# Performance work log

Hardware: AMD Instinct MI355X
Metric: run time of the kernel (lower is better)

The kernel has to match this reference:

```python
import jax, jax.numpy as jnp
import numpy as np
from jax import lax

N_HEAD, D_MODEL, D_HEAD = 8, 128, 16
QLEN, MLEN, BSZ = 1024, 1024, 4
EPS = 1e-6


def _fourier_scores(head_q, head_k, R):
    """Fourier-integral (sinc) attention scores.

    head_q: [qlen, b, H, D], head_k: [klen, b, H, D], R: [H]
    returns [qlen, klen, b, H] = prod_d sin(R*(q_d-k_d))/(q_d-k_d)
    (limit value R when q_d == k_d). Scan over D to avoid a
    [qlen,klen,b,H,D] intermediate.
    """
    qd = jnp.moveaxis(head_q, -1, 0)  # [D, qlen, b, H]
    kd = jnp.moveaxis(head_k, -1, 0)  # [D, klen, b, H]
    init = jnp.ones((head_q.shape[0], head_k.shape[0], head_q.shape[1], R.shape[0]),
                    dtype=head_q.dtype)

    def body(carry, qk):
        q1, k1 = qk  # [qlen,b,H], [klen,b,H]
        diff = q1[:, None, :, :] - k1[None, :, :, :]  # [qlen,klen,b,H]
        small = jnp.abs(diff) < EPS
        safe = jnp.where(small, jnp.ones_like(diff), diff)
        val = jnp.where(small, R, jnp.sin(R * safe) / safe)
        return carry * val, None

    scores, _ = lax.scan(body, init, (qd, kd))
    return scores


def setup_inputs() -> dict:
    key = jax.random.key(0)
    k1, k2, k3, k4, k5 = jax.random.split(key, 5)
    scale = 1.0 / np.sqrt(D_MODEL)
    return {
        "h": jax.random.normal(k1, (QLEN, BSZ, D_MODEL), jnp.float32),
        "mems": jax.random.normal(k2, (MLEN, BSZ, D_MODEL), jnp.float32),
        "Wq": jax.random.normal(k3, (D_MODEL, N_HEAD * D_HEAD), jnp.float32) * scale,
        "Wk": jax.random.normal(k4, (D_MODEL, N_HEAD * D_HEAD), jnp.float32) * scale,
        "paramR": jax.random.normal(k5, (N_HEAD,), jnp.float32),
    }


def reference(h, mems, Wq, Wk, paramR):
    c = jnp.concatenate([mems, h], axis=0)                      # [klen, b, d_model]
    head_q = (h @ Wq).reshape(h.shape[0], h.shape[1], N_HEAD, D_HEAD)
    head_k = (c @ Wk).reshape(c.shape[0], c.shape[1], N_HEAD, D_HEAD)
    scores = _fourier_scores(head_q, head_k, paramR)            # [qlen, klen, b, H]
    return jnp.abs(scores)
```

## Files before the change

### kernel.cpp

```cpp
#include <hip/hip_runtime.h>

#define QLEN 1024
#define KLEN 2048

typedef float f32x2 __attribute__((ext_vector_type(2)));

static constexpr float INV2PI = 0.15915494309189535f;
static constexpr float TGUARD = 3e-5f;

__global__ __launch_bounds__(256) void fa_proj_kernel(
    const float* __restrict__ h, const float* __restrict__ mems,
    const float* __restrict__ Wq, const float* __restrict__ Wk,
    const float* __restrict__ paramR,
    float* __restrict__ Rq3, float* __restrict__ Rk3)
{
    __shared__ float inT[128 * 36];
    const int tid  = threadIdx.x;
    const bool isQ = blockIdx.x < 128;
    const int  blk = isQ ? blockIdx.x : blockIdx.x - 128;
    const int row0 = blk * 32;
    const float* W   = isQ ? Wq : Wk;
    float*      out3 = isQ ? Rq3 : Rk3;

    for (int idx = tid; idx < 32 * 128; idx += 256) {
        int r = idx >> 7;
        int e = idx & 127;
        int grow = row0 + r;
        float v;
        if (isQ)               v = h[(size_t)grow * 128 + e];
        else if (grow < 4096)  v = mems[(size_t)grow * 128 + e];
        else                   v = h[(size_t)(grow - 4096) * 128 + e];
        inT[e * 36 + r] = v;
    }
    __syncthreads();

    const int col  = tid & 127;
    const int half = tid >> 7;

    float acc[16];
#pragma unroll
    for (int j = 0; j < 16; ++j) acc[j] = 0.0f;

#pragma unroll 2
    for (int e = 0; e < 128; ++e) {
        float w = W[e * 128 + col];
        const float4* ap = reinterpret_cast<const float4*>(&inT[e * 36 + half * 16]);
        float4 a0 = ap[0], a1 = ap[1], a2 = ap[2], a3 = ap[3];
        float av[16];
        av[0]=a0.x; av[1]=a0.y; av[2]=a0.z; av[3]=a0.w;
        av[4]=a1.x; av[5]=a1.y; av[6]=a1.z; av[7]=a1.w;
        av[8]=a2.x; av[9]=a2.y; av[10]=a2.z; av[11]=a2.w;
        av[12]=a3.x; av[13]=a3.y; av[14]=a3.z; av[15]=a3.w;
#pragma unroll
        for (int j = 0; j < 16; ++j) acc[j] = fmaf(av[j], w, acc[j]);
    }

    const int hh = col >> 4;
    const int d  = col & 15;
    const float Rrev = paramR[hh] * INV2PI;

#pragma unroll
    for (int j = 0; j < 16; ++j) {
        int r   = row0 + half * 16 + j;
        int tok = r >> 2;
        int b   = r & 3;
        int bh  = b * 8 + hh;
        float p = acc[j];
        float s = __builtin_amdgcn_sinf(Rrev * p);
        float c = __builtin_amdgcn_cosf(Rrev * p);
        int base = ((tok * 12 + (d >> 2)) * 32 + bh) * 4 + (d & 3);
        out3[base]        = p;
        out3[base + 512]  = s;
        out3[base + 1024] = c;
    }
}

__global__ __launch_bounds__(256, 3) void fa_fourier_main(
    const float* __restrict__ Rq3, const float* __restrict__ Rk3,
    const float* __restrict__ paramR, float* __restrict__ out)
{
    __shared__ float4 kbuf[2][1536];

    const int tid   = threadIdx.x;
    const int wv    = tid >> 6;
    const int l     = tid & 63;
    const int dhalf = l >> 5;
    const int bh    = l & 31;
    const int bid   = blockIdx.x;
    const int ch    = bid & 15;
    const int x     = bid >> 4;
    const int k0    = ch * 128;
    const int qb    = x * 16 + wv * 4;

    const float R = paramR[bh & 7];

    f32x2 qp[4][4], qs[4][4], qc[4][4];
    {
        const float4* qsrc = reinterpret_cast<const float4*>(Rq3);
#pragma unroll
        for (int q = 0; q < 4; ++q) {
            size_t tb = (size_t)(qb + q) * 12;
#pragma unroll
            for (int c2 = 0; c2 < 2; ++c2) {
                float4 pv = qsrc[(tb + 0 + dhalf * 2 + c2) * 32 + bh];
                float4 sv = qsrc[(tb + 4 + dhalf * 2 + c2) * 32 + bh];
                float4 cv = qsrc[(tb + 8 + dhalf * 2 + c2) * 32 + bh];
                qp[q][2*c2] = (f32x2){pv.x, pv.y};  qp[q][2*c2+1] = (f32x2){pv.z, pv.w};
                qs[q][2*c2] = (f32x2){sv.x, sv.y};  qs[q][2*c2+1] = (f32x2){sv.z, sv.w};
                qc[q][2*c2] = (f32x2){cv.x, cv.y};  qc[q][2*c2+1] = (f32x2){cv.z, cv.w};
            }
        }
    }

    const float4* ksrc = reinterpret_cast<const float4*>(Rk3);

    float* outA = out + ((size_t)(qb + dhalf * 2) * KLEN + k0) * 32 + bh;
    float* outB = outA + (size_t)KLEN * 32;

    auto stage = [&](int w, int parity) {
        size_t gbase = (size_t)(k0 + w * 4) * 384;
#pragma unroll
        for (int i = 0; i < 6; ++i) {
            int fi = i * 256 + tid;
            __builtin_amdgcn_global_load_lds(
                (const __attribute__((address_space(1))) void*)(ksrc + gbase + fi),
                (__attribute__((address_space(3))) void*)(&kbuf[parity][fi]),
                16, 0, 0);
        }
    };

    stage(0, 0);

    for (int w = 0; w < 32; ++w) {
        __syncthreads();
        if (w < 31) stage(w + 1, (w + 1) & 1);
        const float4* kb = kbuf[w & 1];

#pragma unroll
        for (int t = 0; t < 4; ++t) {
            const float4* kst = kb + t * 384 + bh;
            float4 kpv0 = kst[(0 + dhalf * 2 + 0) * 32];
            float4 kpv1 = kst[(0 + dhalf * 2 + 1) * 32];
            float4 ksv0 = kst[(4 + dhalf * 2 + 0) * 32];
            float4 ksv1 = kst[(4 + dhalf * 2 + 1) * 32];
            float4 kcv0 = kst[(8 + dhalf * 2 + 0) * 32];
            float4 kcv1 = kst[(8 + dhalf * 2 + 1) * 32];
            f32x2 kp2[4] = {{kpv0.x,kpv0.y},{kpv0.z,kpv0.w},{kpv1.x,kpv1.y},{kpv1.z,kpv1.w}};
            f32x2 ks2[4] = {{ksv0.x,ksv0.y},{ksv0.z,ksv0.w},{ksv1.x,ksv1.y},{ksv1.z,ksv1.w}};
            f32x2 kc2[4] = {{kcv0.x,kcv0.y},{kcv0.z,kcv0.w},{kcv1.x,kcv1.y},{kcv1.z,kcv1.w}};

            float rr[4];
#pragma unroll
            for (int q = 0; q < 4; ++q) {
                f32x2 u0 = qp[q][0] - kp2[0];
                f32x2 u1 = qp[q][1] - kp2[1];
                f32x2 u2 = qp[q][2] - kp2[2];
                f32x2 u3 = qp[q][3] - kp2[3];
                f32x2 n0 = __builtin_elementwise_fma(qs[q][0], kc2[0], -(qc[q][0] * ks2[0]));
                f32x2 n1 = __builtin_elementwise_fma(qs[q][1], kc2[1], -(qc[q][1] * ks2[1]));
                f32x2 n2 = __builtin_elementwise_fma(qs[q][2], kc2[2], -(qc[q][2] * ks2[2]));
                f32x2 n3 = __builtin_elementwise_fma(qs[q][3], kc2[3], -(qc[q][3] * ks2[3]));
                f32x2 UU = (u0 * u1) * (u2 * u3);
                f32x2 NN = (n0 * n1) * (n2 * n3);
                float mn = fminf(
                    fminf(fminf(fabsf(u0.x), fabsf(u0.y)), fminf(fabsf(u1.x), fabsf(u1.y))),
                    fminf(fminf(fabsf(u2.x), fabsf(u2.y)), fminf(fabsf(u3.x), fabsf(u3.y))));
                float uh = UU.x * UU.y;
                float nh = NN.x * NN.y;
                if (__builtin_expect(mn < TGUARD, 0)) {
                    float pu = 1.0f, pn = 1.0f;
#pragma unroll
                    for (int j = 0; j < 4; ++j) {
#pragma unroll
                        for (int e = 0; e < 2; ++e) {
                            float u = qp[q][j][e] - kp2[j][e];
                            float n = fmaf(qs[q][j][e], kc2[j][e],
                                           -(qc[q][j][e] * ks2[j][e]));
                            if (fabsf(u) < TGUARD) {
                                float ru = R * u;
                                n = R * fmaf(-ru * ru, 0.16666667f, 1.0f);
                                u = 1.0f;
                            }
                            pu *= u; pn *= n;
                        }
                    }
                    if (fabsf(pu) < 1e-30f) pu = (pu < 0.0f) ? -1e-30f : 1e-30f;
                    uh = pu; nh = pn;
                }
                float uo = __shfl_xor(uh, 32, 64);
                float no = __shfl_xor(nh, 32, 64);
                rr[q] = fabsf((nh * no) * __builtin_amdgcn_rcpf(uh * uo));
            }

            const int t32 = (w * 4 + t) * 32;
            __builtin_nontemporal_store(dhalf ? rr[2] : rr[0], outA + t32);
            __builtin_nontemporal_store(dhalf ? rr[3] : rr[1], outB + t32);
        }
    }
}

extern "C" void kernel_launch(void* const* d_in, const int* in_sizes, int n_in,
                              void* d_out, int out_size, void* d_ws, size_t ws_size,
                              hipStream_t stream)
{
    const float* h    = (const float*)d_in[0];
    const float* mems = (const float*)d_in[1];
    const float* Wq   = (const float*)d_in[2];
    const float* Wk   = (const float*)d_in[3];
    const float* R    = (const float*)d_in[4];
    float* out = (float*)d_out;

    float* Rq3 = (float*)d_ws;
    float* Rk3 = Rq3 + (size_t)1024 * 1536;

    fa_proj_kernel<<<dim3(384), 256, 0, stream>>>(h, mems, Wq, Wk, R, Rq3, Rk3);

    fa_fourier_main<<<dim3(1024), 256, 0, stream>>>(Rq3, Rk3, R, out);
}
```

Measured before the change: 217.9 us.

## Pre-negate q terms, use packed asm math, merge shuffles, rebalance grid

The projection kernel now stores q values and their sines negated, so the main loop can use packed add, mul and fma inline asm without separate negation. The guard check is hoisted so one branch covers all four queries per key. The two shuffles per query are replaced by two per key step by exchanging per-half ratios. The grid shrinks from 1024 to 768 blocks, with uneven key chunks of 172 or 168, likely to fit a single wave of blocks across the CUs. Risks: precision differs slightly because each half-ratio is computed separately, and the inline asm may limit compiler scheduling.

```diff
diff --git a/kernel.cpp b/kernel.cpp
--- a/kernel.cpp
+++ b/kernel.cpp
@@ -7,6 +7,16 @@
 
 static constexpr float INV2PI = 0.15915494309189535f;
 static constexpr float TGUARD = 3e-5f;
+
+static __device__ __forceinline__ f32x2 pk_add(f32x2 a, f32x2 b) {
+    f32x2 d; asm("v_pk_add_f32 %0, %1, %2" : "=v"(d) : "v"(a), "v"(b)); return d;
+}
+static __device__ __forceinline__ f32x2 pk_mul(f32x2 a, f32x2 b) {
+    f32x2 d; asm("v_pk_mul_f32 %0, %1, %2" : "=v"(d) : "v"(a), "v"(b)); return d;
+}
+static __device__ __forceinline__ f32x2 pk_fma(f32x2 a, f32x2 b, f32x2 c) {
+    f32x2 d; asm("v_pk_fma_f32 %0, %1, %2, %3" : "=v"(d) : "v"(a), "v"(b), "v"(c)); return d;
+}
 
 __global__ __launch_bounds__(256) void fa_proj_kernel(
     const float* __restrict__ h, const float* __restrict__ mems,
@@ -21,6 +31,7 @@
     const int row0 = blk * 32;
     const float* W   = isQ ? Wq : Wk;
     float*      out3 = isQ ? Rq3 : Rk3;
+    const float sgn  = isQ ? -1.0f : 1.0f;
 
     for (int idx = tid; idx < 32 * 128; idx += 256) {
         int r = idx >> 7;
@@ -69,8 +80,8 @@
         float s = __builtin_amdgcn_sinf(Rrev * p);
         float c = __builtin_amdgcn_cosf(Rrev * p);
         int base = ((tok * 12 + (d >> 2)) * 32 + bh) * 4 + (d & 3);
-        out3[base]        = p;
-        out3[base + 512]  = s;
+        out3[base]        = sgn * p;
+        out3[base + 512]  = sgn * s;
         out3[base + 1024] = c;
     }
 }
@@ -87,10 +98,14 @@
     const int dhalf = l >> 5;
     const int bh    = l & 31;
     const int bid   = blockIdx.x;
-    const int ch    = bid & 15;
-    const int x     = bid >> 4;
-    const int k0    = ch * 128;
-    const int qb    = x * 16 + wv * 4;
+    const int ch    = bid % 12;
+    const int x     = bid / 12;
+
+    int k0, klen;
+    if (ch < 8) { k0 = ch * 172;              klen = 172; }
+    else        { k0 = 1376 + (ch - 8) * 168; klen = 168; }
+    const int nw = klen >> 2;
+    const int qb = x * 16 + wv * 4;
 
     const float R = paramR[bh & 7];
 
@@ -131,9 +146,9 @@
 
     stage(0, 0);
 
-    for (int w = 0; w < 32; ++w) {
+    for (int w = 0; w < nw; ++w) {
         __syncthreads();
-        if (w < 31) stage(w + 1, (w + 1) & 1);
+        if (w + 1 < nw) stage(w + 1, (w + 1) & 1);
         const float4* kb = kbuf[w & 1];
 
 #pragma unroll
@@ -149,33 +164,44 @@
             f32x2 ks2[4] = {{ksv0.x,ksv0.y},{ksv0.z,ksv0.w},{ksv1.x,ksv1.y},{ksv1.z,ksv1.w}};
             f32x2 kc2[4] = {{kcv0.x,kcv0.y},{kcv0.z,kcv0.w},{kcv1.x,kcv1.y},{kcv1.z,kcv1.w}};
 
-            float rr[4];
+            float g[4];
+            float mnAll = 1e30f;
 #pragma unroll
             for (int q = 0; q < 4; ++q) {
-                f32x2 u0 = qp[q][0] - kp2[0];
-                f32x2 u1 = qp[q][1] - kp2[1];
-                f32x2 u2 = qp[q][2] - kp2[2];
-                f32x2 u3 = qp[q][3] - kp2[3];
-                f32x2 n0 = __builtin_elementwise_fma(qs[q][0], kc2[0], -(qc[q][0] * ks2[0]));
-                f32x2 n1 = __builtin_elementwise_fma(qs[q][1], kc2[1], -(qc[q][1] * ks2[1]));
-                f32x2 n2 = __builtin_elementwise_fma(qs[q][2], kc2[2], -(qc[q][2] * ks2[2]));
-                f32x2 n3 = __builtin_elementwise_fma(qs[q][3], kc2[3], -(qc[q][3] * ks2[3]));
-                f32x2 UU = (u0 * u1) * (u2 * u3);
-                f32x2 NN = (n0 * n1) * (n2 * n3);
-                float mn = fminf(
+                f32x2 u0 = pk_add(qp[q][0], kp2[0]);
+                f32x2 u1 = pk_add(qp[q][1], kp2[1]);
+                f32x2 u2 = pk_add(qp[q][2], kp2[2]);
+                f32x2 u3 = pk_add(qp[q][3], kp2[3]);
+                f32x2 t0 = pk_mul(qs[q][0], kc2[0]);
+                f32x2 t1 = pk_mul(qs[q][1], kc2[1]);
+                f32x2 t2 = pk_mul(qs[q][2], kc2[2]);
+                f32x2 t3 = pk_mul(qs[q][3], kc2[3]);
+                f32x2 n0 = pk_fma(qc[q][0], ks2[0], t0);
+                f32x2 n1 = pk_fma(qc[q][1], ks2[1], t1);
+                f32x2 n2 = pk_fma(qc[q][2], ks2[2], t2);
+                f32x2 n3 = pk_fma(qc[q][3], ks2[3], t3);
+                f32x2 UU = pk_mul(pk_mul(u0, u1), pk_mul(u2, u3));
+                f32x2 NN = pk_mul(pk_mul(n0, n1), pk_mul(n2, n3));
+                float uh = UU.x * UU.y;
+                float nh = NN.x * NN.y;
+                g[q] = nh * __builtin_amdgcn_rcpf(uh);
+                float m = fminf(
                     fminf(fminf(fabsf(u0.x), fabsf(u0.y)), fminf(fabsf(u1.x), fabsf(u1.y))),
                     fminf(fminf(fabsf(u2.x), fabsf(u2.y)), fminf(fabsf(u3.x), fabsf(u3.y))));
-                float uh = UU.x * UU.y;
-                float nh = NN.x * NN.y;
-                if (__builtin_expect(mn < TGUARD, 0)) {
+                mnAll = fminf(mnAll, m);
+            }
+
+            if (__builtin_expect(mnAll < TGUARD, 0)) {
+#pragma unroll
+                for (int q = 0; q < 4; ++q) {
                     float pu = 1.0f, pn = 1.0f;
 #pragma unroll
                     for (int j = 0; j < 4; ++j) {
 #pragma unroll
                         for (int e = 0; e < 2; ++e) {
-                            float u = qp[q][j][e] - kp2[j][e];
-                            float n = fmaf(qs[q][j][e], kc2[j][e],
-                                           -(qc[q][j][e] * ks2[j][e]));
+                            float u = qp[q][j][e] + kp2[j][e];
+                            float n = fmaf(qc[q][j][e], ks2[j][e],
+                                           qs[q][j][e] * kc2[j][e]);
                             if (fabsf(u) < TGUARD) {
                                 float ru = R * u;
                                 n = R * fmaf(-ru * ru, 0.16666667f, 1.0f);
@@ -185,16 +211,20 @@
                         }
                     }
                     if (fabsf(pu) < 1e-30f) pu = (pu < 0.0f) ? -1e-30f : 1e-30f;
-                    uh = pu; nh = pn;
+                    g[q] = pn * __builtin_amdgcn_rcpf(pu);
                 }
-                float uo = __shfl_xor(uh, 32, 64);
-                float no = __shfl_xor(nh, 32, 64);
-                rr[q] = fabsf((nh * no) * __builtin_amdgcn_rcpf(uh * uo));
             }
 
+            float sendA = dhalf ? g[0] : g[2];
+            float sendB = dhalf ? g[1] : g[3];
+            float recvA = __shfl_xor(sendA, 32, 64);
+            float recvB = __shfl_xor(sendB, 32, 64);
+            float myA   = dhalf ? g[2] : g[0];
+            float myB   = dhalf ? g[3] : g[1];
+
             const int t32 = (w * 4 + t) * 32;
-            __builtin_nontemporal_store(dhalf ? rr[2] : rr[0], outA + t32);
-            __builtin_nontemporal_store(dhalf ? rr[3] : rr[1], outB + t32);
+            __builtin_nontemporal_store(fabsf(myA * recvA), outA + t32);
+            __builtin_nontemporal_store(fabsf(myB * recvB), outB + t32);
         }
     }
 }
@@ -215,5 +245,5 @@
 
     fa_proj_kernel<<<dim3(384), 256, 0, stream>>>(h, mems, Wq, Wk, R, Rq3, Rk3);
 
-    fa_fourier_main<<<dim3(1024), 256, 0, stream>>>(Rq3, Rk3, R, out);
-}
+    fa_fourier_main<<<dim3(768), 256, 0, stream>>>(Rq3, Rk3, R, out);
+}
```

New measurement: 325.0 us. 1.49x slower.
